# Kernel tuning notes

Measured on AMD Instinct MI355X. Metric: run time of the kernel, lower is better.

## Reference

```python
import jax, jax.numpy as jnp
import numpy as np
from jax.scipy.special import logsumexp

EPS = 0.1
NITS = 50
TOL = 1e-3


def pairwise_sqdist(x, y):
    # x: (B, n, d), y: (B, m, d) -> (B, n, m) squared euclidean distances
    rx = jnp.sum(x * x, axis=-1)[:, :, None]
    ry = jnp.sum(y * y, axis=-1)[:, None, :]
    return rx + ry - 2.0 * jnp.einsum('bnd,bmd->bnm', x, y)


def sink_transport(C, alpha_log, beta_log, eps=EPS, nits=NITS, tol=TOL):
    # Entropic-OT Sinkhorn in log domain; mirrors torch `sink` (no_grad).
    # C: (B, n, n); alpha_log: (B, n, 1); beta_log: (B, n, 1)
    B, n, m = C.shape
    Ce = -C / eps                      # (B, n, m)
    Cet = jnp.swapaxes(Ce, 1, 2)       # (B, m, n)
    A0 = jnp.zeros((B, m, 1), C.dtype)
    B0 = jnp.zeros((B, n, 1), C.dtype)
    big = jnp.asarray(jnp.inf, C.dtype)

    def cond(state):
        _, _, i, a_err, b_err = state
        return (i < nits) & ((a_err >= tol) | (b_err >= tol))

    def body(state):
        A_j, B_i, i, _, _ = state
        A_new = -logsumexp(B_i + alpha_log + Ce, axis=1, keepdims=True)
        A_new = jnp.swapaxes(A_new, 1, 2)          # (B, m, 1)
        B_new = -logsumexp(A_new + beta_log + Cet, axis=1, keepdims=True)
        B_new = jnp.swapaxes(B_new, 1, 2)          # (B, n, 1)
        b_err = jnp.max(eps * jnp.mean(jnp.abs(B_i - B_new), axis=1)[:, 0])
        a_err = jnp.max(eps * jnp.mean(jnp.abs(A_j - A_new), axis=1)[:, 0])
        return (A_new, B_new, i + 1, a_err, b_err)

    A_j, B_i, _, _, _ = jax.lax.while_loop(cond, body, (A0, B0, jnp.int32(0), big, big))
    transp = jnp.exp(jnp.swapaxes(A_j, 1, 2) + B_i - C / eps) / (n * m)
    return transp


def setup_inputs() -> dict:
    key = jax.random.key(0)
    k1, k2 = jax.random.split(key)
    preds = jax.random.normal(k1, (4, 2048, 3), dtype=jnp.float32)
    gts = jax.random.normal(k2, (4, 2048, 3), dtype=jnp.float32)
    return {"preds": preds, "gts": gts}


def reference(preds, gts):
    B, N, _ = preds.shape
    M = gts.shape[1]
    # C[b, i, j] = ||gts[b,i] - preds[b,j]||^2   (rows = gt, cols = pred)
    C = pairwise_sqdist(gts, preds)            # (B, M, N)
    Cd = jax.lax.stop_gradient(C)

    # Chamfer (computed on detached C in the original)
    loss_1 = jnp.mean(jnp.min(Cd, axis=1), axis=1)
    loss_2 = jnp.mean(jnp.min(Cd, axis=2), axis=1)
    chamfer_loss = jnp.mean(loss_1 + loss_2)

    # Weights: note original uses 1/batch_size (faithful to source)
    alpha_log = jnp.log(jnp.full((B, N, 1), 1.0 / B, dtype=preds.dtype))
    beta_log = jnp.log(jnp.full((B, M, 1), 1.0 / B, dtype=preds.dtype))

    transp = sink_transport(Cd, alpha_log, beta_log)
    cost = jnp.sum(transp * C, axis=(1, 2))

    # Entropy correction: W(p, q) - 1/2 W(p, p)
    C_correct = pairwise_sqdist(preds, preds)  # (B, N, N)
    transp_c = sink_transport(jax.lax.stop_gradient(C_correct), alpha_log, alpha_log)
    cost_correct = jnp.sum(transp_c * C_correct, axis=(1, 2))
    cost = cost - 0.5 * cost_correct
    return cost, chamfer_loss
```

## Files before the change

### kernel.cpp

```cpp
#include <hip/hip_runtime.h>

#define NPTS 2048
#define NB 4
#define NITS 50
#define TOLC 1e-3f
#define EPSC 0.1f
#define INV_EPS 10.0f
#define LAC (-1.3862943611198906f)
#define L2E 1.4426950408889634f
#define LN2C 0.6931471805599453f
#define KS (L2E*2.0f*INV_EPS)
#define CSTRIDE 16

#define OFF_A 0
#define OFF_B 32768
#define OFF_ERR 65536
#define OFF_COST 66336
#define OFF_CHAM 66344
#define OFF_BARC 66352
#define OFF_DONE 66480
#define ZERO_FLOATS 66496

__device__ __forceinline__ float wsum(float v) {
#pragma unroll
  for (int o = 32; o; o >>= 1) v += __shfl_xor(v, o, 64);
  return v;
}

__device__ __forceinline__ float aload(const float* p) {
  return __hip_atomic_load(p, __ATOMIC_RELAXED, __HIP_MEMORY_SCOPE_AGENT);
}
__device__ __forceinline__ void astore(float* p, float v) {
  __hip_atomic_store(p, v, __ATOMIC_RELAXED, __HIP_MEMORY_SCOPE_AGENT);
}

__device__ __forceinline__ void pbar(unsigned* c, unsigned target) {
  __syncthreads();
  if (threadIdx.x == 0) {
    __builtin_amdgcn_s_waitcnt(0);
    __hip_atomic_fetch_add(c, 1u, __ATOMIC_RELAXED, __HIP_MEMORY_SCOPE_AGENT);
    while (__hip_atomic_load(c, __ATOMIC_RELAXED, __HIP_MEMORY_SCOPE_AGENT) < target)
      __builtin_amdgcn_s_sleep(1);
  }
  __syncthreads();
}

__global__ __launch_bounds__(256) void chamfer_k(const float* __restrict__ preds,
                                                 const float* __restrict__ gts,
                                                 float* __restrict__ ws) {
  __shared__ float4 colv[NPTS];
  int dir = blockIdx.x >> 5;
  int b = (blockIdx.x >> 3) & 3;
  int chunk = blockIdx.x & 7;
  const float* rowP = dir ? preds : gts;
  const float* colP = dir ? gts : preds;
  for (int c = threadIdx.x; c < NPTS; c += 256) {
    const float* p = colP + (b * NPTS + c) * 3;
    colv[c] = make_float4(p[0], p[1], p[2], p[0]*p[0] + p[1]*p[1] + p[2]*p[2]);
  }
  __syncthreads();
  int r = chunk * 256 + threadIdx.x;
  const float* p = rowP + (b * NPTS + r) * 3;
  float rn = p[0]*p[0] + p[1]*p[1] + p[2]*p[2];
  float nx = -2.f*p[0], ny = -2.f*p[1], nz = -2.f*p[2];
  float mn = 1e30f;
  for (int c = 0; c < NPTS; ++c) {
    float4 v = colv[c];
    float t = fmaf(nx, v.x, fmaf(ny, v.y, fmaf(nz, v.z, v.w)));
    mn = fminf(mn, t);
  }
  mn += rn;
  mn = wsum(mn);
  if ((threadIdx.x & 63) == 0) atomicAdd(ws + OFF_CHAM, mn * (1.0f/8192.0f));
}

__device__ __forceinline__ void half_update(const float4* __restrict__ svL,
    const float* __restrict__ potSrc, const float* __restrict__ oPts,
    const float4* __restrict__ oCw, const float* __restrict__ oPrev,
    float* __restrict__ oNew, float* __restrict__ errSlot,
    int blk, int tid, float* __restrict__ pot, float (*comb)[64]) {
  pot[tid]        = aload(potSrc + tid);
  pot[tid + 1024] = aload(potSrc + tid + 1024);
  __syncthreads();
  const int wave = tid >> 6, lane = tid & 63;
  const int ih = wave >> 3, jq = wave & 7;
  const int o0 = blk * 64 + jq * 8;
  float y0[8], y1[8], y2[8], S[8], s[8];
#pragma unroll
  for (int q = 0; q < 8; ++q) {
    int o = o0 + q;
    y0[q] = oPts[o*3+0]; y1[q] = oPts[o*3+1]; y2[q] = oPts[o*3+2];
    float c = LAC + oCw[o].w * LN2C;
    S[q] = L2E * (-aload(&oPrev[o]) - c);
    s[q] = 0.f;
  }
  const float4* basep = svL + ih * 1024;
  const float* potp = pot + ih * 1024;
#pragma unroll 2
  for (int stp = 0; stp < 16; ++stp) {
    int il = stp * 64 + lane;
    float4 v = basep[il];
    float wv = fmaf(L2E, potp[il], v.w);
#pragma unroll
    for (int q = 0; q < 8; ++q) {
      float m = wv - S[q];
      m = fmaf(v.x, y0[q], m);
      m = fmaf(v.y, y1[q], m);
      m = fmaf(v.z, y2[q], m);
      s[q] += __builtin_amdgcn_exp2f(m);
    }
  }
#pragma unroll
  for (int q = 0; q < 8; ++q) s[q] = wsum(s[q]);
  if (lane == 0) {
#pragma unroll
    for (int q = 0; q < 8; ++q) comb[ih][jq * 8 + q] = s[q];
  }
  __syncthreads();
  if (tid < 64) {
    int o = blk * 64 + tid;
    float stot = fmaxf(comb[0][tid] + comb[1][tid], 1e-38f);
    float c = LAC + oCw[o].w * LN2C;
    float pv = aload(&oPrev[o]);
    float Sv = L2E * (-pv - c);
    float nv = -c - LN2C * (__builtin_amdgcn_logf(stot) + Sv);
    float d = fabsf(nv - pv);
    astore(&oNew[o], nv);
    d = wsum(d);
    if (tid == 0) atomicAdd(errSlot, d);
  }
  __syncthreads();
}

__global__ __launch_bounds__(1024, 4) void sink_k(const float* __restrict__ preds,
    const float* __restrict__ gts, float* __restrict__ ws, float* __restrict__ out) {
  __shared__ float4 svR[NPTS];
  __shared__ float4 svC[NPTS];
  __shared__ float pot[NPTS];
  __shared__ float comb[2][64];
  __shared__ int decS;
  const int p = blockIdx.x & 7;
  const int blk = blockIdx.x >> 3;
  const int b = p & 3;
  const int g = p >> 2;
  const bool fs = (g == 0);
  const int tid = threadIdx.x;

  const float* colPts = preds + b * NPTS * 3;
  const float* rowPts = fs ? gts + b * NPTS * 3 : colPts;

  for (int i = tid; i < NPTS; i += 1024) {
    const float* q3 = rowPts + i * 3;
    float x = q3[0], y = q3[1], z = q3[2];
    svR[i] = make_float4(KS*x, KS*y, KS*z, -L2E*INV_EPS*(x*x + y*y + z*z));
    const float* c3 = colPts + i * 3;
    float cx = c3[0], cy = c3[1], cz = c3[2];
    svC[i] = make_float4(KS*cx, KS*cy, KS*cz, -L2E*INV_EPS*(cx*cx + cy*cy + cz*cz));
  }

  float* Abase = ws + OFF_A;
  float* Bbase = ws + OFF_B;
  float* err = ws + OFF_ERR;
  unsigned* ub = reinterpret_cast<unsigned*>(ws);
  unsigned* barc = ub + OFF_BARC;
  unsigned* mybar = barc + p * CSTRIDE;
  unsigned* done = ub + OFF_DONE;
  const float sc = EPSC / (float)NPTS;

  int last = NITS - 1;
  for (int it = 0; it <= NITS; ++it) {
    const int w = it & 1, r = 1 - (it & 1);
    if (tid == 0) {
      int dec = 1;
      if (it >= 2) {
        unsigned need = 32u * (2u * (unsigned)it - 2u);
        for (;;) {
          unsigned mn = 0xFFFFFFFFu;
#pragma unroll
          for (int q = 0; q < 4; ++q) {
            unsigned v = __hip_atomic_load(barc + (g*4 + q) * CSTRIDE,
                                           __ATOMIC_RELAXED, __HIP_MEMORY_SCOPE_AGENT);
            mn = v < mn ? v : mn;
          }
          if (mn >= need) break;
          __builtin_amdgcn_s_sleep(1);
        }
        int j = it - 2;
        float ae = 0.f, be = 0.f;
#pragma unroll
        for (int q = 0; q < 4; ++q) {
          ae = fmaxf(ae, aload(err + ((j*8 + g*4 + q)*2 + 0)));
          be = fmaxf(be, aload(err + ((j*8 + g*4 + q)*2 + 1)));
        }
        if (!((sc*ae >= TOLC) || (sc*be >= TOLC))) dec = 0;
      }
      decS = dec;
    }
    __syncthreads();
    if (decS == 0) { last = it - 2; break; }
    if (it == NITS) { last = NITS - 1; break; }
    half_update(svR, Bbase + r*16384 + p*NPTS, colPts, svC,
                Abase + r*16384 + p*NPTS, Abase + w*16384 + p*NPTS,
                err + ((it*8 + p)*2 + 0), blk, tid, pot, comb);
    pbar(mybar, 32u * (2u*(unsigned)it + 1u));
    half_update(svC, Abase + w*16384 + p*NPTS, rowPts, svR,
                Bbase + r*16384 + p*NPTS, Bbase + w*16384 + p*NPTS,
                err + ((it*8 + p)*2 + 1), blk, tid, pot, comb);
    pbar(mybar, 32u * (2u*(unsigned)it + 2u));
    last = it;
  }

  {
    const float* Af = Abase + (last & 1)*16384 + p*NPTS;
    const float* Bf = Bbase + (last & 1)*16384 + p*NPTS;
    pot[tid]        = aload(Bf + tid);
    pot[tid + 1024] = aload(Bf + tid + 1024);
    __syncthreads();
    const int wave = tid >> 6, lane = tid & 63;
    const int ih = wave >> 3, jq = wave & 7;
    const int j0 = blk * 64 + jq * 8;
    float y0[8], y1[8], y2[8], Q[8], EA[8];
#pragma unroll
    for (int q = 0; q < 8; ++q) {
      int j = j0 + q;
      y0[q] = colPts[j*3+0]; y1[q] = colPts[j*3+1]; y2[q] = colPts[j*3+2];
      float aj = aload(Af + j);
      Q[q] = L2E * aj + svC[j].w;
      EA[q] = EPSC * aj;
    }
    float acc = 0.f;
    const float4* basep = svR + ih * 1024;
    const float* potp = pot + ih * 1024;
#pragma unroll 2
    for (int stp = 0; stp < 16; ++stp) {
      int il = stp * 64 + lane;
      float4 v = basep[il];
      float pw = potp[il];
      float wv = fmaf(L2E, pw, v.w);
      float eb = EPSC * pw;
#pragma unroll
      for (int q = 0; q < 8; ++q) {
        float m = wv + Q[q];
        m = fmaf(v.x, y0[q], m);
        m = fmaf(v.y, y1[q], m);
        m = fmaf(v.z, y2[q], m);
        float e = __builtin_amdgcn_exp2f(m);
        float Cv = fmaf(-(EPSC*LN2C), m, eb + EA[q]);
        acc = fmaf(e, Cv, acc);
      }
    }
    acc = wsum(acc);
    if (lane == 0) atomicAdd(ws + OFF_COST + p, acc);
  }

  __syncthreads();
  if (tid == 0) {
    __builtin_amdgcn_s_waitcnt(0);
    __hip_atomic_fetch_add(done, 1u, __ATOMIC_RELAXED, __HIP_MEMORY_SCOPE_AGENT);
  }
  if (blockIdx.x == 0) {
    if (tid == 0) {
      while (__hip_atomic_load(done, __ATOMIC_RELAXED, __HIP_MEMORY_SCOPE_AGENT) < 256u)
        __builtin_amdgcn_s_sleep(1);
    }
    __syncthreads();
    if (tid < 4)
      out[tid] = (aload(ws + OFF_COST + tid) - 0.5f * aload(ws + OFF_COST + 4 + tid)) *
                 (1.0f / ((float)NPTS * (float)NPTS));
    if (tid == 4) out[4] = aload(ws + OFF_CHAM);
  }
}

extern "C" void kernel_launch(void* const* d_in, const int* in_sizes, int n_in,
                              void* d_out, int out_size, void* d_ws, size_t ws_size,
                              hipStream_t stream) {
  const float* preds = (const float*)d_in[0];
  const float* gts   = (const float*)d_in[1];
  float* wsf  = (float*)d_ws;
  float* outf = (float*)d_out;

  hipMemsetAsync(d_ws, 0, ZERO_FLOATS * sizeof(float), stream);
  chamfer_k<<<64, 256, 0, stream>>>(preds, gts, wsf);

  void* args[] = { (void*)&preds, (void*)&gts, (void*)&wsf, (void*)&outf };
  hipLaunchCooperativeKernel((void*)sink_k, dim3(256), dim3(1024), args, 0, stream);
}
```

Before: 1.156 ms.

## Replace atomic-counter grid barrier with per-block flag barrier

Replaces the shared atomic fetch-add counter barrier between the 32 blocks of each problem with per-block flag slots. Each block stores its own epoch value and one wavefront polls all 32 flags in parallel, reducing the minimum with shuffles. The convergence check also polls 128 flags with one wave instead of 4 counters serially. This is meant to remove atomic contention and serialized polling latency on a barrier hit twice per Sinkhorn iteration, at the cost of more polling loads and a larger workspace region.

New measurement: 1.145 ms. About the same (-0.9%).

```diff
diff --git a/kernel.cpp b/kernel.cpp
--- a/kernel.cpp
+++ b/kernel.cpp
@@ -17,9 +17,9 @@
 #define OFF_ERR 65536
 #define OFF_COST 66336
 #define OFF_CHAM 66344
-#define OFF_BARC 66352
-#define OFF_DONE 66480
-#define ZERO_FLOATS 66496
+#define OFF_FLAG 66352
+#define OFF_DONE 70448
+#define ZERO_FLOATS 70464
 
 __device__ __forceinline__ float wsum(float v) {
 #pragma unroll
@@ -33,14 +33,31 @@
 __device__ __forceinline__ void astore(float* p, float v) {
   __hip_atomic_store(p, v, __ATOMIC_RELAXED, __HIP_MEMORY_SCOPE_AGENT);
 }
-
-__device__ __forceinline__ void pbar(unsigned* c, unsigned target) {
-  __syncthreads();
-  if (threadIdx.x == 0) {
-    __builtin_amdgcn_s_waitcnt(0);
-    __hip_atomic_fetch_add(c, 1u, __ATOMIC_RELAXED, __HIP_MEMORY_SCOPE_AGENT);
-    while (__hip_atomic_load(c, __ATOMIC_RELAXED, __HIP_MEMORY_SCOPE_AGENT) < target)
-      __builtin_amdgcn_s_sleep(1);
+__device__ __forceinline__ unsigned uload(const unsigned* p) {
+  return __hip_atomic_load(p, __ATOMIC_RELAXED, __HIP_MEMORY_SCOPE_AGENT);
+}
+
+__device__ __forceinline__ void fbar(unsigned* fl, int blk, unsigned target) {
+  __syncthreads();
+  if (threadIdx.x < 64) {
+    if (threadIdx.x == 0) {
+      __builtin_amdgcn_s_waitcnt(0);
+      __hip_atomic_store(fl + blk * CSTRIDE, target,
+                         __ATOMIC_RELAXED, __HIP_MEMORY_SCOPE_AGENT);
+    }
+    unsigned mn;
+    do {
+      unsigned v = 0xFFFFFFFFu;
+      if (threadIdx.x < 32)
+        v = (threadIdx.x == (unsigned)blk) ? target
+            : uload(fl + threadIdx.x * CSTRIDE);
+      mn = v;
+#pragma unroll
+      for (int o = 32; o; o >>= 1) {
+        unsigned t = __shfl_xor(mn, o, 64);
+        mn = t < mn ? t : mn;
+      }
+    } while (mn < target);
   }
   __syncthreads();
 }
@@ -162,51 +179,53 @@
   float* Bbase = ws + OFF_B;
   float* err = ws + OFF_ERR;
   unsigned* ub = reinterpret_cast<unsigned*>(ws);
-  unsigned* barc = ub + OFF_BARC;
-  unsigned* mybar = barc + p * CSTRIDE;
+  unsigned* flags = ub + OFF_FLAG;
+  unsigned* myfl = flags + p * 32 * CSTRIDE;
   unsigned* done = ub + OFF_DONE;
   const float sc = EPSC / (float)NPTS;
 
   int last = NITS - 1;
   for (int it = 0; it <= NITS; ++it) {
     const int w = it & 1, r = 1 - (it & 1);
-    if (tid == 0) {
-      int dec = 1;
-      if (it >= 2) {
-        unsigned need = 32u * (2u * (unsigned)it - 2u);
+    if (it >= 2) {
+      if (tid < 64) {
+        unsigned need = 2u * (unsigned)it - 2u;
+        const unsigned* gfl = flags + g * 128 * CSTRIDE;
         for (;;) {
-          unsigned mn = 0xFFFFFFFFu;
-#pragma unroll
-          for (int q = 0; q < 4; ++q) {
-            unsigned v = __hip_atomic_load(barc + (g*4 + q) * CSTRIDE,
-                                           __ATOMIC_RELAXED, __HIP_MEMORY_SCOPE_AGENT);
-            mn = v < mn ? v : mn;
+          unsigned v0 = uload(gfl + tid * CSTRIDE);
+          unsigned v1 = uload(gfl + (64 + tid) * CSTRIDE);
+          unsigned mn = v0 < v1 ? v0 : v1;
+#pragma unroll
+          for (int o = 32; o; o >>= 1) {
+            unsigned t = __shfl_xor(mn, o, 64);
+            mn = t < mn ? t : mn;
           }
           if (mn >= need) break;
-          __builtin_amdgcn_s_sleep(1);
+          __builtin_amdgcn_s_sleep(2);
         }
-        int j = it - 2;
-        float ae = 0.f, be = 0.f;
-#pragma unroll
-        for (int q = 0; q < 4; ++q) {
-          ae = fmaxf(ae, aload(err + ((j*8 + g*4 + q)*2 + 0)));
-          be = fmaxf(be, aload(err + ((j*8 + g*4 + q)*2 + 1)));
+        if (tid == 0) {
+          int j = it - 2;
+          float ae = 0.f, be = 0.f;
+#pragma unroll
+          for (int q = 0; q < 4; ++q) {
+            ae = fmaxf(ae, aload(err + ((j*8 + g*4 + q)*2 + 0)));
+            be = fmaxf(be, aload(err + ((j*8 + g*4 + q)*2 + 1)));
+          }
+          decS = ((sc*ae >= TOLC) || (sc*be >= TOLC)) ? 1 : 0;
         }
-        if (!((sc*ae >= TOLC) || (sc*be >= TOLC))) dec = 0;
       }
-      decS = dec;
-    }
-    __syncthreads();
-    if (decS == 0) { last = it - 2; break; }
+      __syncthreads();
+      if (decS == 0) { last = it - 2; break; }
+    }
     if (it == NITS) { last = NITS - 1; break; }
     half_update(svR, Bbase + r*16384 + p*NPTS, colPts, svC,
                 Abase + r*16384 + p*NPTS, Abase + w*16384 + p*NPTS,
                 err + ((it*8 + p)*2 + 0), blk, tid, pot, comb);
-    pbar(mybar, 32u * (2u*(unsigned)it + 1u));
+    fbar(myfl, blk, 2u*(unsigned)it + 1u);
     half_update(svC, Abase + w*16384 + p*NPTS, rowPts, svR,
                 Bbase + r*16384 + p*NPTS, Bbase + w*16384 + p*NPTS,
                 err + ((it*8 + p)*2 + 1), blk, tid, pot, comb);
-    pbar(mybar, 32u * (2u*(unsigned)it + 2u));
+    fbar(myfl, blk, 2u*(unsigned)it + 2u);
     last = it;
   }
 
```
